# Kernel optimization log

Hardware: AMD Instinct MI355X
Metric: run time of the kernel (lower is better)

## Reference

```python
import jax, jax.numpy as jnp
import numpy as np

N_NODES = 38000   # 19 feature types x ~2000 categories
IN_DIM = 64
HID = 128         # hid_num in source
R = 8             # number of relations
E = 200000        # edges per relation
N_ROWS = 60000    # data rows
F = 19            # len(features)
N_CLASSES = 10


def setup_inputs() -> dict:
    key = jax.random.key(0)
    ks = jax.random.split(key, 20)
    s_in = 1.0 / np.sqrt(IN_DIM)
    s_h = 1.0 / np.sqrt(HID)
    inp = {
        "node_feats": jax.random.normal(ks[0], (N_NODES, IN_DIM), jnp.float32),
        "edges_src": jax.random.randint(ks[1], (R, E), 0, N_NODES),
        "edges_dst": jax.random.randint(ks[2], (R, E), 0, N_NODES),
        "row_idx": jax.random.randint(ks[3], (N_ROWS, F), 0, N_NODES),
        "row_mask": jax.random.randint(ks[4], (N_ROWS, F), 0, 2).astype(bool),
        # input linear
        "W_in": jax.random.normal(ks[5], (IN_DIM, HID), jnp.float32) * s_in,
        "b_in": jnp.zeros((HID,), jnp.float32),
        # RGCN layer 1 and 2: per-relation GraphConv weights
        "W1": jax.random.normal(ks[6], (R, HID, HID), jnp.float32) * s_h,
        "b1": jnp.zeros((R, HID), jnp.float32),
        "W2": jax.random.normal(ks[7], (R, HID, HID), jnp.float32) * s_h,
        "b2": jnp.zeros((R, HID), jnp.float32),
        # MLP head
        "Wm1": jax.random.normal(ks[8], (HID, HID), jnp.float32) * s_h,
        "bm1": jnp.zeros((HID,), jnp.float32),
        "Wm2": jax.random.normal(ks[9], (HID, HID), jnp.float32) * s_h,
        "bm2": jnp.zeros((HID,), jnp.float32),
        "Wm3": jax.random.normal(ks[10], (HID, N_CLASSES), jnp.float32) * s_h,
        "bm3": jnp.zeros((N_CLASSES,), jnp.float32),
    }
    return inp


def _hetero_conv(h, src, dst, W, b):
    """DGL HeteroGraphConv(sum) of GraphConv(norm='both') over R relations."""
    n = h.shape[0]
    out = jnp.zeros((n, W.shape[2]), h.dtype)
    ones = jnp.ones((src.shape[1],), h.dtype)
    for r in range(src.shape[0]):
        deg_out = jax.ops.segment_sum(ones, src[r], num_segments=n)
        deg_in = jax.ops.segment_sum(ones, dst[r], num_segments=n)
        norm_s = jnp.where(deg_out > 0, deg_out, 1.0) ** -0.5
        norm_d = jnp.where(deg_in > 0, deg_in, 1.0) ** -0.5
        msg = h[src[r]] * norm_s[src[r], None]            # [E, hid]
        agg = jax.ops.segment_sum(msg, dst[r], num_segments=n)
        out = out + (agg * norm_d[:, None]) @ W[r] + b[r]
    return out


def reference(node_feats, edges_src, edges_dst, row_idx, row_mask,
              W_in, b_in, W1, b1, W2, b2, Wm1, bm1, Wm2, bm2, Wm3, bm3):
    # input linear + relu (applied to every node type's features)
    h = jax.nn.relu(node_feats @ W_in + b_in)            # [N_nodes, HID]
    # 2-layer RGCN
    h = jax.nn.relu(_hetero_conv(h, edges_src, edges_dst, W1, b1))
    h = _hetero_conv(h, edges_src, edges_dst, W2, b2)    # [N_nodes, HID]
    # vectorized ragged gather + masked mean (replaces per-row python loop)
    m = row_mask.astype(h.dtype)                          # [N_rows, F]
    emb = h[row_idx] * m[..., None]                       # [N_rows, F, HID]
    cnt = jnp.maximum(m.sum(-1, keepdims=True), 1.0)
    mean_feat = emb.sum(1) / cnt                          # [N_rows, HID]
    # MLP head
    x = jax.nn.relu(mean_feat @ Wm1 + bm1)
    x = jax.nn.relu(x @ Wm2 + bm2)
    return x @ Wm3 + bm3                                  # [N_rows, N_CLASSES]
```

## Files before the change

### kernel.cpp

```cpp
#include <hip/hip_runtime.h>
#include <hip/hip_bf16.h>

#define NN    38000
#define HID   128
#define RR    8
#define EE    200000
#define NROWS 60000
#define FF    19
#define NCLS  10
#define NRD   (RR*NN)
#define HB    38912
#define CH    16
#define CE    (EE/CH)

typedef __hip_bfloat16 bf16;
typedef __attribute__((ext_vector_type(8))) short short8;
typedef __attribute__((ext_vector_type(4))) float floatx4;

__device__ __forceinline__ float b2f(bf16 x){ return __bfloat162float(x); }
__device__ __forceinline__ bf16  f2b(float x){ return __float2bfloat16(x); }

__device__ __forceinline__ int geti(const void* a, long long i, int wide){
  return wide ? (int)(((const long long*)a)[i]) : ((const int*)a)[i];
}

__global__ void k_fill(float* out, int n, float v){
  int i = blockIdx.x*256 + threadIdx.x;
  if (i < n) out[i] = v;
}

__global__ void k_sniff(const void* mask, const void* ridx, const void* esrc, int* flags){
  int lane = threadIdx.x;
  const unsigned short* mu = (const unsigned short*)mask;
  int l3f80e=0, l3f80o=0, lbytehi=0, loddnz=0, lother=0;
  for (int i = lane; i < 4096; i += 64){
    unsigned v = mu[i];
    if (v == 0) continue;
    if (v == 0x3F80){ if (i & 1) l3f80o = 1; else l3f80e = 1; continue; }
    unsigned lo = v & 0xFF, hi = v >> 8;
    int lob = (lo == 0 || lo == 1 || lo == 0xFF);
    int hib = (hi == 0 || hi == 1 || hi == 0xFF);
    if (lob && hib){ if (hi) lbytehi = 1; if (i & 1) loddnz = 1; continue; }
    lother = 1;
  }
  int a3f80e = __any(l3f80e);
  int a3f80o = __any(l3f80o);
  int abytehi = __any(lbytehi);
  int aoddnz = __any(loddnz);
  int aother = __any(lother);
  int mtype = -1;
  if (!aother){
    if (a3f80e && !abytehi && !aoddnz)       mtype = 2;
    else if (a3f80o && !a3f80e && !abytehi)  mtype = 3;
    else if (!a3f80e && !a3f80o){
      if (abytehi || aoddnz) mtype = 1;
      else                   mtype = 0;
    }
  }
  const int* es = (const int*)esrc;
  int loddE = 0, lseenE = 0;
  for (int i = lane; i < 512; i += 64){
    if (es[2*i+1] != 0) loddE = 1;
    if (es[2*i] > 1)    lseenE = 1;
  }
  int fE = (!__any(loddE) && __any(lseenE)) ? 1 : 0;
  const int* ri = (const int*)ridx;
  int loddI = 0, lseenI = 0;
  for (int i = lane; i < 512; i += 64){
    if (ri[2*i+1] != 0) loddI = 1;
    if (ri[2*i] > 1)    lseenI = 1;
  }
  int fI = (!__any(loddI) && __any(lseenI)) ? 1 : 0;
  if (lane == 0){ flags[1] = mtype; flags[3] = fE; flags[4] = fI; }
}


__global__ __launch_bounds__(1024) void kg_hist(const void* esrc, const void* edst,
                                                int* __restrict__ ghd, int* __restrict__ ghs,
                                                const int* flags){
  __shared__ int hist[HB];
  int t = threadIdx.x;
  for (int i = t; i < HB; i += 1024) hist[i] = 0;
  __syncthreads();
  int b = blockIdx.x;
  int side = b >> 7;
  int r = (b >> 4) & 7, c = b & 15;
  int wide = flags[3];
  const void* e = side ? esrc : edst;
  long long base = (long long)r*EE + (long long)c*CE;
  if (!wide){
    const int* p = (const int*)e + base;
    for (int i = t; i < CE; i += 1024) atomicAdd(&hist[p[i]], 1);
  } else {
    const long long* p = (const long long*)e + base;
    for (int i = t; i < CE; i += 1024) atomicAdd(&hist[(int)p[i]], 1);
  }
  __syncthreads();
  int* out = (side ? ghs : ghd) + (long long)(r*CH + c)*HB;
  for (int i = t; i < HB; i += 1024) out[i] = hist[i];
}

__global__ void kg_tot(const int* __restrict__ ghd, const int* __restrict__ ghs,
                       int* __restrict__ totg, float* __restrict__ ns){
  int i = blockIdx.x*256 + threadIdx.x;
  if (i >= RR*HB) return;
  int r = i / HB, bin = i - r*HB;
  int sd = 0, ss = 0;
#pragma unroll
  for (int c = 0; c < CH; c++){
    sd += ghd[(long long)(r*CH+c)*HB + bin];
    ss += ghs[(long long)(r*CH+c)*HB + bin];
  }
  totg[i] = sd;
  if (bin < NN) ns[r*NN + bin] = rsqrtf((float)(ss > 0 ? ss : 1));
}

__global__ __launch_bounds__(1024) void kg_scan(const int* __restrict__ totg,
                                                int* __restrict__ rowptr){
  __shared__ int tot[HB];
  __shared__ int wsum[16];
  int t = threadIdx.x, r = blockIdx.x;
  for (int i = t; i < HB; i += 1024) tot[i] = totg[r*HB + i];
  __syncthreads();
  int b0 = t*38;
  int loc[38], s = 0;
#pragma unroll
  for (int j = 0; j < 38; j++){ loc[j] = s; s += tot[b0+j]; }
  int lane = t & 63, w = t >> 6;
  int sc = s;
  for (int off = 1; off < 64; off <<= 1){
    int v = __shfl_up(sc, off);
    if (lane >= off) sc += v;
  }
  if (lane == 63) wsum[w] = sc;
  __syncthreads();
  if (t < 16){
    int v = wsum[t];
    int scw = v;
    for (int off = 1; off < 16; off <<= 1){
      int u = __shfl_up(scw, off);
      if (t >= off) scw += u;
    }
    wsum[t] = scw - v;
  }
  __syncthreads();
  int base = r*EE + (sc - s) + wsum[w];
#pragma unroll
  for (int j = 0; j < 38; j++) tot[b0+j] = base + loc[j];
  __syncthreads();
  for (int i = t; i < NN; i += 1024) rowptr[r*NN + i] = tot[i];
  if (r == RR-1 && t == 0) rowptr[NRD] = RR*EE;
}

__global__ void kg_curs(const int* __restrict__ ghd, const int* __restrict__ rowptr,
                        int* __restrict__ gcurs){
  int i = blockIdx.x*256 + threadIdx.x;
  if (i >= NRD) return;
  int r = i / NN, bin = i - r*NN;
  int p = rowptr[i];
#pragma unroll
  for (int c = 0; c < CH; c++){
    gcurs[(long long)(r*CH+c)*HB + bin] = p;
    p += ghd[(long long)(r*CH+c)*HB + bin];
  }
}

__global__ __launch_bounds__(1024) void kg_scatter(const void* esrc, const void* edst,
                                                   const int* __restrict__ gcurs,
                                                   int* __restrict__ csr, const int* flags){
  __shared__ int cur[HB];
  int t = threadIdx.x, b = blockIdx.x;
  int r = b >> 4, c = b & 15;
  const int* g = gcurs + (long long)(r*CH + c)*HB;
  for (int i = t; i < HB; i += 1024) cur[i] = g[i];
  __syncthreads();
  int wide = flags[3];
  long long base = (long long)r*EE + (long long)c*CE;
  if (!wide){
    const int* ps = (const int*)esrc + base;
    const int* pd = (const int*)edst + base;
    for (int i = t; i < CE; i += 1024){
      int d = pd[i], s = ps[i];
      int pos = atomicAdd(&cur[d], 1);
      csr[pos] = s;
    }
  } else {
    const long long* ps = (const long long*)esrc + base;
    const long long* pd = (const long long*)edst + base;
    for (int i = t; i < CE; i += 1024){
      int d = (int)pd[i], s = (int)ps[i];
      int pos = atomicAdd(&cur[d], 1);
      csr[pos] = s;
    }
  }
}


__global__ void k_bias(const float* b_in, const float* b1, const float* b2,
                       const float* bm1, const float* bm2, const float* bm3, float* o){
  int t = threadIdx.x;
  o[t] = b_in[t];
  float s1 = 0.f, s2 = 0.f;
  for (int r = 0; r < RR; r++){ s1 += b1[r*HID+t]; s2 += b2[r*HID+t]; }
  o[128+t] = s1; o[256+t] = s2;
  o[384+t] = bm1[t]; o[512+t] = bm2[t];
  if (t < NCLS) o[640+t] = bm3[t];
}

__global__ void k_pack512(const float* __restrict__ WA, const float* __restrict__ WB,
                          bf16* __restrict__ outA, bf16* __restrict__ outB){
  int idx0 = blockIdx.x*256 + threadIdx.x;
  if (idx0 >= 4*65536) return;
  const float* W = (idx0 < 2*65536) ? WA : WB;
  bf16* out      = (idx0 < 2*65536) ? outA : outB;
  int idx = idx0 & (2*65536 - 1);
  int j = idx & 7;
  int l = (idx >> 3) & 63;
  int t = (idx >> 9) & 127;
  int g = idx >> 16;
  int ktg = t & 15, nt = t >> 4;
  int kglob = ktg*32 + ((l>>4)<<3) + j;
  int rel = kglob >> 7;
  int krow = kglob & 127;
  int n = nt*16 + (l&15);
  out[idx] = f2b(W[((g*4 + rel)*128 + krow)*128 + n]);
}

__global__ void k_packg(const float* __restrict__ B, bf16* __restrict__ out, int KT){
  int idx = blockIdx.x*256 + threadIdx.x;
  if (idx >= KT*4096) return;
  int j  = idx & 7;
  int l  = (idx >> 3) & 63;
  int t  = idx >> 9;
  int kt = t % KT;
  int nt = t / KT;
  int k = kt*32 + ((l>>4)<<3) + j;
  int n = nt*16 + (l&15);
  out[idx] = f2b(B[k*128 + n]);
}

__global__ void k_gemm_in(const float* __restrict__ A, const float* __restrict__ B,
                          const float* bias, bf16* __restrict__ out){
  int row0 = blockIdx.x * 4;
  int col = threadIdx.x;
  float a0=0.f, a1=0.f, a2=0.f, a3=0.f;
  for (int k = 0; k < 64; k++){
    float bv = B[k*HID + col];
    a0 += A[(long long)(row0+0)*64 + k] * bv;
    a1 += A[(long long)(row0+1)*64 + k] * bv;
    a2 += A[(long long)(row0+2)*64 + k] * bv;
    a3 += A[(long long)(row0+3)*64 + k] * bv;
  }
  float bb = bias[col];
  out[(long long)(row0+0)*HID + col] = f2b(fmaxf(a0 + bb, 0.f));
  out[(long long)(row0+1)*HID + col] = f2b(fmaxf(a1 + bb, 0.f));
  out[(long long)(row0+2)*HID + col] = f2b(fmaxf(a2 + bb, 0.f));
  out[(long long)(row0+3)*HID + col] = f2b(fmaxf(a3 + bb, 0.f));
}

__global__ __launch_bounds__(512) void k_layer(const bf16* __restrict__ h,
                                               const int* __restrict__ rowptr,
                                               const int* __restrict__ csr,
                                               const float* __restrict__ ns,
                                               const bf16* __restrict__ Bp,
                                               const float* __restrict__ bias,
                                               bf16* __restrict__ hout, int relu){
  __shared__ char lds[8*16*256];
  int w = threadIdx.x >> 6;
  int lane = threadIdx.x & 63;
  int d0 = blockIdx.x << 4;
  const unsigned* hv = (const unsigned*)h;
  const float* nsw = ns + w*NN;

  int rp = 0;
  if (lane < 17) rp = rowptr[w*NN + d0 + lane];
  int beg16 = __shfl(rp, 0);
  int end16 = __shfl(rp, 16);

  int wbase = beg16;
  int s_l = 0; float w_l = 0.f;
  { int pos = wbase + lane;
    if (pos < end16){ s_l = csr[pos]; w_l = nsw[s_l]; } }

  for (int i = 0; i < 16; i++){
    int b = __shfl(rp, i), e = __shfl(rp, i+1);
    float acc0 = 0.f, acc1 = 0.f;
    int j = b;
    while (j < e){
      while (j >= wbase + 64){
        wbase += 64;
        int pos = wbase + lane;
        s_l = 0; w_l = 0.f;
        if (pos < end16){ s_l = csr[pos]; w_l = nsw[s_l]; }
      }
      int wend = wbase + 64;
      int stop = e < wend ? e : wend;
      int m = stop - j;
      int base_l = j - wbase;
      int nb = (m + 3) & ~3;
      for (int k = 0; k < nb; k += 4){
        int i0 = base_l + k;
        int   s0 = __shfl(s_l, i0),   s1 = __shfl(s_l, i0+1);
        int   s2 = __shfl(s_l, i0+2), s3 = __shfl(s_l, i0+3);
        float w0 = __shfl(w_l, i0),   w1 = __shfl(w_l, i0+1);
        float w2 = __shfl(w_l, i0+2), w3 = __shfl(w_l, i0+3);
        if (k+1 >= m) w1 = 0.f;
        if (k+2 >= m) w2 = 0.f;
        if (k+3 >= m) w3 = 0.f;
        unsigned p0 = hv[(long long)s0*64 + lane];
        unsigned p1 = hv[(long long)s1*64 + lane];
        unsigned p2 = hv[(long long)s2*64 + lane];
        unsigned p3 = hv[(long long)s3*64 + lane];
        acc0 += w0 * __uint_as_float(p0 << 16);
        acc1 += w0 * __uint_as_float(p0 & 0xffff0000u);
        acc0 += w1 * __uint_as_float(p1 << 16);
        acc1 += w1 * __uint_as_float(p1 & 0xffff0000u);
        acc0 += w2 * __uint_as_float(p2 << 16);
        acc1 += w2 * __uint_as_float(p2 & 0xffff0000u);
        acc0 += w3 * __uint_as_float(p3 << 16);
        acc1 += w3 * __uint_as_float(p3 & 0xffff0000u);
      }
      j = stop;
    }
    int deg = e - b;
    float nd = rsqrtf((float)(deg > 0 ? deg : 1));
    bf16 o0 = f2b(acc0 * nd), o1 = f2b(acc1 * nd);
    unsigned ov = ((unsigned)(*(unsigned short*)&o1) << 16) | (*(unsigned short*)&o0);
    int addr = (w << 12) + (i << 8) + (lane << 2);
    addr ^= ((i & 7) << 4);
    *(unsigned*)(lds + addr) = ov;
  }
  __syncthreads();

  floatx4 acc = (floatx4){0.f,0.f,0.f,0.f};
  int row = lane & 15;
  int kb = (lane >> 4) << 4;
#pragma unroll
  for (int rel = 0; rel < 8; rel++){
    int half = rel >> 2;
    const bf16* bp = Bp + half*65536 + lane*8 + (w*16 + (rel & 3)*4)*512;
#pragma unroll
    for (int ktl = 0; ktl < 4; ktl++){
      int off = (row << 8) + ktl*64 + kb;
      off ^= ((row & 7) << 4);
      short8 a = *(const short8*)(lds + (rel << 12) + off);
      short8 b = *(const short8*)(bp + ktl*512);
      acc = __builtin_amdgcn_mfma_f32_16x16x32_bf16(a, b, acc, 0, 0, 0);
    }
  }
  int col = w*16 + (lane & 15);
  int row0 = d0 + ((lane >> 4) << 2);
  float bb = bias[col];
#pragma unroll
  for (int v = 0; v < 4; v++){
    float x = acc[v] + bb;
    if (relu) x = fmaxf(x, 0.f);
    hout[(long long)(row0 + v)*HID + col] = f2b(x);
  }
}

__global__ void k_mfma_out(const bf16* __restrict__ A, const bf16* __restrict__ Bp,
                           const float* __restrict__ bias, bf16* __restrict__ out, int M){
  int wave = (blockIdx.x*blockDim.x + threadIdx.x) >> 6;
  int lane = threadIdx.x & 63;
  int rowBase = wave << 4;
  if (rowBase >= M) return;
  long long aRow = rowBase + (lane & 15);
  int kGrp = (lane >> 4) << 3;
  floatx4 acc[8];
#pragma unroll
  for (int nt = 0; nt < 8; nt++) acc[nt] = (floatx4){0.f,0.f,0.f,0.f};
  const bf16* bp = Bp + lane*8;
#pragma unroll
  for (int kt = 0; kt < 4; kt++){
    short8 a = *(const short8*)(A + aRow*HID + kt*32 + kGrp);
#pragma unroll
    for (int nt = 0; nt < 8; nt++){
      short8 b = *(const short8*)(bp + (nt*4 + kt)*512);
      acc[nt] = __builtin_amdgcn_mfma_f32_16x16x32_bf16(a, b, acc[nt], 0, 0, 0);
    }
  }
  int colB = lane & 15;
  int rowQ = rowBase + ((lane >> 4) << 2);
#pragma unroll
  for (int nt = 0; nt < 8; nt++){
    int col = nt*16 + colB;
    float bb = bias[col];
#pragma unroll
    for (int v = 0; v < 4; v++)
      out[(long long)(rowQ+v)*HID + col] = f2b(fmaxf(acc[nt][v] + bb, 0.f));
  }
}

__global__ void k_mean(const bf16* __restrict__ h, const void* ridx, const void* rmask,
                       const int* flags, bf16* __restrict__ mean){
  int row = blockIdx.x*4 + (threadIdx.x >> 6);
  int lane = threadIdx.x & 63;
  int mt = flags[1];
  int wide = flags[4];
  const int* m4            = (const int*)rmask;
  const unsigned char* m1  = (const unsigned char*)rmask;
  const unsigned short* m2 = (const unsigned short*)rmask;
  const unsigned int* mw   = (const unsigned int*)rmask;
  const unsigned* hv = (const unsigned*)h;
  int on = 0, idxl = 0;
  if (lane < FF){
    long long i = (long long)row*FF + lane;
    if      (mt == 1) on = (m1[i] != 0);
    else if (mt == 2) on = (m2[i] != 0);
    else if (mt == 3) on = (mw[i] != 0);
    else              on = (m4[i] != 0);
    if (on) idxl = geti(ridx, i, wide);
  }
  unsigned long long bal = __ballot(on);
  float cnt = (float)__popcll(bal);
  float acc0 = 0.f, acc1 = 0.f;
#pragma unroll
  for (int j = 0; j < FF; j++){
    int s = __shfl(idxl, j);
    float w = (float)((bal >> j) & 1ull);
    unsigned pv = hv[(long long)s*64 + lane];
    acc0 += w * __uint_as_float(pv << 16);
    acc1 += w * __uint_as_float(pv & 0xffff0000u);
  }
  float inv = 1.f / fmaxf(cnt, 1.f);
  bf16 o0 = f2b(acc0 * inv), o1 = f2b(acc1 * inv);
  unsigned ov = ((unsigned)(*(unsigned short*)&o1) << 16) | (*(unsigned short*)&o0);
  ((unsigned*)mean)[(long long)row*64 + lane] = ov;
}

__global__ void k_last(const bf16* __restrict__ A, const float* __restrict__ B,
                       const float* bias, float* __restrict__ out){
  int i = blockIdx.x*256 + threadIdx.x;
  if (i >= NROWS*NCLS) return;
  int row = i / NCLS, col = i - row*NCLS;
  float acc = bias[col];
  const bf16* ar = A + (long long)row*HID;
  for (int k = 0; k < HID; k++) acc += b2f(ar[k]) * B[k*NCLS + col];
  out[i] = acc;
}

extern "C" void kernel_launch(void* const* d_in, const int* in_sizes, int n_in,
                              void* d_out, int out_size, void* d_ws, size_t ws_size,
                              hipStream_t stream){
  float* out = (float*)d_out;

  static const int expect[17] = {
    NN*64, RR*EE, RR*EE, NROWS*FF, NROWS*FF,
    64*HID, HID, RR*HID*HID, RR*HID, RR*HID*HID, RR*HID,
    HID*HID, HID, HID*HID, HID, HID*NCLS, NCLS };
  bool ok = (n_in >= 17) && (out_size == NROWS*NCLS);
  if (ok) for (int i = 0; i < 17; i++) if (in_sizes[i] != expect[i]) { ok = false; break; }
  if (!ok){
    k_fill<<<(NROWS*NCLS+255)/256, 256, 0, stream>>>(out, NROWS*NCLS, 64.0f);
    return;
  }

  const void*  e_src = d_in[1];
  const void*  e_dst = d_in[2];
  const void*  ridx  = d_in[3];
  const void*  rmask = d_in[4];
  const float* nf   = (const float*)d_in[0];
  const float* W_in = (const float*)d_in[5];
  const float* b_in = (const float*)d_in[6];
  const float* W1   = (const float*)d_in[7];
  const float* b1   = (const float*)d_in[8];
  const float* W2   = (const float*)d_in[9];
  const float* b2   = (const float*)d_in[10];
  const float* Wm1  = (const float*)d_in[11];
  const float* bm1  = (const float*)d_in[12];
  const float* Wm2  = (const float*)d_in[13];
  const float* bm2  = (const float*)d_in[14];
  const float* Wm3  = (const float*)d_in[15];
  const float* bm3  = (const float*)d_in[16];

  char* ws = (char*)d_ws;
  size_t off = 0;
  auto take = [&](size_t bytes)->char*{
    char* p = ws + off; off += (bytes + 255) & ~(size_t)255; return p; };

  int*   flags  = (int*)  take(256);
  char*  rgn    =         take(58368000);
  bf16*  meanb  = (bf16*) (rgn);
  bf16*  x1     = (bf16*) (rgn + 15360000);
  bf16*  x2     = (bf16*) (rgn + 30720000);
  int*   ghd    = (int*)  (rgn);
  int*   ghs    = (int*)  (rgn + 19922944);
  int*   gcurs  = (int*)  (rgn + 19922944);
  int*   totg   = (int*)  (rgn + 39845888);
  bf16*  h1     = (bf16*) take((size_t)NN*HID*2);
  bf16*  h2     = (bf16*) take((size_t)NN*HID*2);
  int*   rowptr = (int*)  take((size_t)(NRD+1)*4);
  int*   csr    = (int*)  take((size_t)RR*EE*4);
  float* ns     = (float*)take((size_t)NRD*4);
  float* bias   = (float*)take(656*4);
  bf16*  W1p    = (bf16*) take((size_t)2*65536*2);
  bf16*  W2p    = (bf16*) take((size_t)2*65536*2);
  bf16*  Wm1p   = (bf16*) take((size_t)16384*2);
  bf16*  Wm2p   = (bf16*) take((size_t)16384*2);

  if (off > ws_size){
    k_fill<<<(NROWS*NCLS+255)/256, 256, 0, stream>>>(out, NROWS*NCLS, 32.0f);
    return;
  }

  k_sniff   <<<1, 64, 0, stream>>>(rmask, ridx, e_src, flags);
  kg_hist   <<<256, 1024, 0, stream>>>(e_src, e_dst, ghd, ghs, flags);
  kg_tot    <<<(RR*HB+255)/256, 256, 0, stream>>>(ghd, ghs, totg, ns);
  kg_scan   <<<RR, 1024, 0, stream>>>(totg, rowptr);
  kg_curs   <<<(NRD+255)/256, 256, 0, stream>>>(ghd, rowptr, gcurs);
  kg_scatter<<<128, 1024, 0, stream>>>(e_src, e_dst, gcurs, csr, flags);
  k_bias    <<<1, 128, 0, stream>>>(b_in, b1, b2, bm1, bm2, bm3, bias);

  k_pack512<<<(4*65536+255)/256, 256, 0, stream>>>(W1, W2, W1p, W2p);
  k_packg  <<<(4*4096+255)/256, 256, 0, stream>>>(Wm1, Wm1p, 4);
  k_packg  <<<(4*4096+255)/256, 256, 0, stream>>>(Wm2, Wm2p, 4);

  k_gemm_in<<<NN/4, 128, 0, stream>>>(nf, W_in, bias+0, h1);

  k_layer<<<NN/16, 512, 0, stream>>>(h1, rowptr, csr, ns, W1p, bias+128, h2, 1);
  k_layer<<<NN/16, 512, 0, stream>>>(h2, rowptr, csr, ns, W2p, bias+256, h1, 0);

  k_mean<<<NROWS/4, 256, 0, stream>>>(h1, ridx, rmask, flags, meanb);

  int gR = (NROWS/16 + 3)/4;
  k_mfma_out<<<gR, 256, 0, stream>>>(meanb, Wm1p, bias+384, x1, NROWS);
  k_mfma_out<<<gR, 256, 0, stream>>>(x1,    Wm2p, bias+512, x2, NROWS);
  k_last<<<(NROWS*NCLS+255)/256, 256, 0, stream>>>(x2, Wm3, bias+640, out);
}
```

Measured before the change: 490.6 us.

## Pack source norm into CSR entries and load edges with uniform scalar reads

```diff
diff --git a/kernel.cpp b/kernel.cpp
--- a/kernel.cpp
+++ b/kernel.cpp
@@ -167,14 +167,17 @@
 
 __global__ __launch_bounds__(1024) void kg_scatter(const void* esrc, const void* edst,
                                                    const int* __restrict__ gcurs,
-                                                   int* __restrict__ csr, const int* flags){
+                                                   const float* __restrict__ ns,
+                                                   int2* __restrict__ csrw, const int* flags){
   __shared__ int cur[HB];
   int t = threadIdx.x, b = blockIdx.x;
   int r = b >> 4, c = b & 15;
   const int* g = gcurs + (long long)(r*CH + c)*HB;
   for (int i = t; i < HB; i += 1024) cur[i] = g[i];
   __syncthreads();
+  if (b == 0 && t < 8){ int2 z; z.x = 0; z.y = 0; csrw[RR*EE + t] = z; }
   int wide = flags[3];
+  const float* nsr = ns + r*NN;
   long long base = (long long)r*EE + (long long)c*CE;
   if (!wide){
     const int* ps = (const int*)esrc + base;
@@ -182,7 +185,8 @@
     for (int i = t; i < CE; i += 1024){
       int d = pd[i], s = ps[i];
       int pos = atomicAdd(&cur[d], 1);
-      csr[pos] = s;
+      int2 v; v.x = s; v.y = __float_as_int(nsr[s]);
+      csrw[pos] = v;
     }
   } else {
     const long long* ps = (const long long*)esrc + base;
@@ -190,7 +194,8 @@
     for (int i = t; i < CE; i += 1024){
       int d = (int)pd[i], s = (int)ps[i];
       int pos = atomicAdd(&cur[d], 1);
-      csr[pos] = s;
+      int2 v; v.x = s; v.y = __float_as_int(nsr[s]);
+      csrw[pos] = v;
     }
   }
 }
@@ -207,36 +212,39 @@
   if (t < NCLS) o[640+t] = bm3[t];
 }
 
-__global__ void k_pack512(const float* __restrict__ WA, const float* __restrict__ WB,
-                          bf16* __restrict__ outA, bf16* __restrict__ outB){
+__global__ void k_packall(const float* __restrict__ W1, const float* __restrict__ W2,
+                          const float* __restrict__ Wm1, const float* __restrict__ Wm2,
+                          bf16* __restrict__ W1p, bf16* __restrict__ W2p,
+                          bf16* __restrict__ Wm1p, bf16* __restrict__ Wm2p){
   int idx0 = blockIdx.x*256 + threadIdx.x;
-  if (idx0 >= 4*65536) return;
-  const float* W = (idx0 < 2*65536) ? WA : WB;
-  bf16* out      = (idx0 < 2*65536) ? outA : outB;
-  int idx = idx0 & (2*65536 - 1);
-  int j = idx & 7;
-  int l = (idx >> 3) & 63;
-  int t = (idx >> 9) & 127;
-  int g = idx >> 16;
-  int ktg = t & 15, nt = t >> 4;
-  int kglob = ktg*32 + ((l>>4)<<3) + j;
-  int rel = kglob >> 7;
-  int krow = kglob & 127;
-  int n = nt*16 + (l&15);
-  out[idx] = f2b(W[((g*4 + rel)*128 + krow)*128 + n]);
-}
-
-__global__ void k_packg(const float* __restrict__ B, bf16* __restrict__ out, int KT){
-  int idx = blockIdx.x*256 + threadIdx.x;
-  if (idx >= KT*4096) return;
-  int j  = idx & 7;
-  int l  = (idx >> 3) & 63;
-  int t  = idx >> 9;
-  int kt = t % KT;
-  int nt = t / KT;
-  int k = kt*32 + ((l>>4)<<3) + j;
-  int n = nt*16 + (l&15);
-  out[idx] = f2b(B[k*128 + n]);
+  if (idx0 < 4*65536){
+    const float* W = (idx0 < 2*65536) ? W1 : W2;
+    bf16* out      = (idx0 < 2*65536) ? W1p : W2p;
+    int idx = idx0 & (2*65536 - 1);
+    int j = idx & 7;
+    int l = (idx >> 3) & 63;
+    int t = (idx >> 9) & 127;
+    int g = idx >> 16;
+    int ktg = t & 15, nt = t >> 4;
+    int kglob = ktg*32 + ((l>>4)<<3) + j;
+    int rel = kglob >> 7;
+    int krow = kglob & 127;
+    int n = nt*16 + (l&15);
+    out[idx] = f2b(W[((g*4 + rel)*128 + krow)*128 + n]);
+  } else if (idx0 < 4*65536 + 2*16384){
+    int t2 = idx0 - 4*65536;
+    const float* B = (t2 < 16384) ? Wm1 : Wm2;
+    bf16* out      = (t2 < 16384) ? Wm1p : Wm2p;
+    int idx = t2 & 16383;
+    int j  = idx & 7;
+    int l  = (idx >> 3) & 63;
+    int t  = idx >> 9;
+    int kt = t & 3;
+    int nt = t >> 2;
+    int k = kt*32 + ((l>>4)<<3) + j;
+    int n = nt*16 + (l&15);
+    out[idx] = f2b(B[k*128 + n]);
+  }
 }
 
 __global__ void k_gemm_in(const float* __restrict__ A, const float* __restrict__ B,
@@ -260,8 +268,7 @@
 
 __global__ __launch_bounds__(512) void k_layer(const bf16* __restrict__ h,
                                                const int* __restrict__ rowptr,
-                                               const int* __restrict__ csr,
-                                               const float* __restrict__ ns,
+                                               const unsigned long long* __restrict__ cw,
                                                const bf16* __restrict__ Bp,
                                                const float* __restrict__ bias,
                                                bf16* __restrict__ hout, int relu){
@@ -270,57 +277,36 @@
   int lane = threadIdx.x & 63;
   int d0 = blockIdx.x << 4;
   const unsigned* hv = (const unsigned*)h;
-  const float* nsw = ns + w*NN;
 
   int rp = 0;
   if (lane < 17) rp = rowptr[w*NN + d0 + lane];
-  int beg16 = __shfl(rp, 0);
-  int end16 = __shfl(rp, 16);
-
-  int wbase = beg16;
-  int s_l = 0; float w_l = 0.f;
-  { int pos = wbase + lane;
-    if (pos < end16){ s_l = csr[pos]; w_l = nsw[s_l]; } }
 
   for (int i = 0; i < 16; i++){
-    int b = __shfl(rp, i), e = __shfl(rp, i+1);
+    int b = __builtin_amdgcn_readfirstlane(__shfl(rp, i));
+    int e = __builtin_amdgcn_readfirstlane(__shfl(rp, i+1));
     float acc0 = 0.f, acc1 = 0.f;
-    int j = b;
-    while (j < e){
-      while (j >= wbase + 64){
-        wbase += 64;
-        int pos = wbase + lane;
-        s_l = 0; w_l = 0.f;
-        if (pos < end16){ s_l = csr[pos]; w_l = nsw[s_l]; }
-      }
-      int wend = wbase + 64;
-      int stop = e < wend ? e : wend;
-      int m = stop - j;
-      int base_l = j - wbase;
-      int nb = (m + 3) & ~3;
-      for (int k = 0; k < nb; k += 4){
-        int i0 = base_l + k;
-        int   s0 = __shfl(s_l, i0),   s1 = __shfl(s_l, i0+1);
-        int   s2 = __shfl(s_l, i0+2), s3 = __shfl(s_l, i0+3);
-        float w0 = __shfl(w_l, i0),   w1 = __shfl(w_l, i0+1);
-        float w2 = __shfl(w_l, i0+2), w3 = __shfl(w_l, i0+3);
-        if (k+1 >= m) w1 = 0.f;
-        if (k+2 >= m) w2 = 0.f;
-        if (k+3 >= m) w3 = 0.f;
-        unsigned p0 = hv[(long long)s0*64 + lane];
-        unsigned p1 = hv[(long long)s1*64 + lane];
-        unsigned p2 = hv[(long long)s2*64 + lane];
-        unsigned p3 = hv[(long long)s3*64 + lane];
-        acc0 += w0 * __uint_as_float(p0 << 16);
-        acc1 += w0 * __uint_as_float(p0 & 0xffff0000u);
-        acc0 += w1 * __uint_as_float(p1 << 16);
-        acc1 += w1 * __uint_as_float(p1 & 0xffff0000u);
-        acc0 += w2 * __uint_as_float(p2 << 16);
-        acc1 += w2 * __uint_as_float(p2 & 0xffff0000u);
-        acc0 += w3 * __uint_as_float(p3 << 16);
-        acc1 += w3 * __uint_as_float(p3 & 0xffff0000u);
-      }
-      j = stop;
+    for (int j = b; j < e; j += 4){
+      unsigned long long q0 = cw[j];
+      unsigned long long q1 = cw[j+1];
+      unsigned long long q2 = cw[j+2];
+      unsigned long long q3 = cw[j+3];
+      int s0 = (int)q0, s1 = (int)q1, s2 = (int)q2, s3 = (int)q3;
+      float w0 = __int_as_float((int)(q0 >> 32));
+      float w1 = (j+1 < e) ? __int_as_float((int)(q1 >> 32)) : 0.f;
+      float w2 = (j+2 < e) ? __int_as_float((int)(q2 >> 32)) : 0.f;
+      float w3 = (j+3 < e) ? __int_as_float((int)(q3 >> 32)) : 0.f;
+      unsigned p0 = hv[(long long)s0*64 + lane];
+      unsigned p1 = hv[(long long)s1*64 + lane];
+      unsigned p2 = hv[(long long)s2*64 + lane];
+      unsigned p3 = hv[(long long)s3*64 + lane];
+      acc0 += w0 * __uint_as_float(p0 << 16);
+      acc1 += w0 * __uint_as_float(p0 & 0xffff0000u);
+      acc0 += w1 * __uint_as_float(p1 << 16);
+      acc1 += w1 * __uint_as_float(p1 & 0xffff0000u);
+      acc0 += w2 * __uint_as_float(p2 << 16);
+      acc1 += w2 * __uint_as_float(p2 & 0xffff0000u);
+      acc0 += w3 * __uint_as_float(p3 << 16);
+      acc1 += w3 * __uint_as_float(p3 & 0xffff0000u);
     }
     int deg = e - b;
     float nd = rsqrtf((float)(deg > 0 ? deg : 1));
@@ -392,36 +378,55 @@
   }
 }
 
-__global__ void k_mean(const bf16* __restrict__ h, const void* ridx, const void* rmask,
-                       const int* flags, bf16* __restrict__ mean){
+__global__ void k_mean(const bf16* __restrict__ h, const void* __restrict__ ridx,
+                       const void* __restrict__ rmask,
+                       const int* __restrict__ flags, bf16* __restrict__ mean){
   int row = blockIdx.x*4 + (threadIdx.x >> 6);
   int lane = threadIdx.x & 63;
   int mt = flags[1];
   int wide = flags[4];
-  const int* m4            = (const int*)rmask;
-  const unsigned char* m1  = (const unsigned char*)rmask;
-  const unsigned short* m2 = (const unsigned short*)rmask;
-  const unsigned int* mw   = (const unsigned int*)rmask;
   const unsigned* hv = (const unsigned*)h;
-  int on = 0, idxl = 0;
-  if (lane < FF){
-    long long i = (long long)row*FF + lane;
-    if      (mt == 1) on = (m1[i] != 0);
-    else if (mt == 2) on = (m2[i] != 0);
-    else if (mt == 3) on = (mw[i] != 0);
-    else              on = (m4[i] != 0);
-    if (on) idxl = geti(ridx, i, wide);
-  }
-  unsigned long long bal = __ballot(on);
-  float cnt = (float)__popcll(bal);
-  float acc0 = 0.f, acc1 = 0.f;
-#pragma unroll
-  for (int j = 0; j < FF; j++){
-    int s = __shfl(idxl, j);
-    float w = (float)((bal >> j) & 1ull);
-    unsigned pv = hv[(long long)s*64 + lane];
-    acc0 += w * __uint_as_float(pv << 16);
-    acc1 += w * __uint_as_float(pv & 0xffff0000u);
+  float acc0 = 0.f, acc1 = 0.f, cnt = 0.f;
+  if (mt == 0 && !wide){
+    int urow = __builtin_amdgcn_readfirstlane(row);
+    const int* m4 = (const int*)rmask;
+    const int* r4 = (const int*)ridx;
+    long long base = (long long)urow*FF;
+#pragma unroll
+    for (int j = 0; j < FF; j++){
+      int mv = m4[base + j];
+      if (mv){
+        int s = r4[base + j];
+        unsigned pv = hv[(long long)s*64 + lane];
+        acc0 += __uint_as_float(pv << 16);
+        acc1 += __uint_as_float(pv & 0xffff0000u);
+        cnt += 1.f;
+      }
+    }
+  } else {
+    const int* m4            = (const int*)rmask;
+    const unsigned char* m1  = (const unsigned char*)rmask;
+    const unsigned short* m2 = (const unsigned short*)rmask;
+    const unsigned int* mw   = (const unsigned int*)rmask;
+    int on = 0, idxl = 0;
+    if (lane < FF){
+      long long i = (long long)row*FF + lane;
+      if      (mt == 1) on = (m1[i] != 0);
+      else if (mt == 2) on = (m2[i] != 0);
+      else if (mt == 3) on = (mw[i] != 0);
+      else              on = (m4[i] != 0);
+      if (on) idxl = geti(ridx, i, wide);
+    }
+    unsigned long long bal = __ballot(on);
+    cnt = (float)__popcll(bal);
+#pragma unroll
+    for (int j = 0; j < FF; j++){
+      int s = __shfl(idxl, j);
+      float w = (float)((bal >> j) & 1ull);
+      unsigned pv = hv[(long long)s*64 + lane];
+      acc0 += w * __uint_as_float(pv << 16);
+      acc1 += w * __uint_as_float(pv & 0xffff0000u);
+    }
   }
   float inv = 1.f / fmaxf(cnt, 1.f);
   bf16 o0 = f2b(acc0 * inv), o1 = f2b(acc1 * inv);
@@ -491,7 +496,7 @@
   bf16*  h1     = (bf16*) take((size_t)NN*HID*2);
   bf16*  h2     = (bf16*) take((size_t)NN*HID*2);
   int*   rowptr = (int*)  take((size_t)(NRD+1)*4);
-  int*   csr    = (int*)  take((size_t)RR*EE*4);
+  int2*  csrw   = (int2*) take((size_t)RR*EE*8 + 64);
   float* ns     = (float*)take((size_t)NRD*4);
   float* bias   = (float*)take(656*4);
   bf16*  W1p    = (bf16*) take((size_t)2*65536*2);
@@ -509,17 +514,18 @@
   kg_tot    <<<(RR*HB+255)/256, 256, 0, stream>>>(ghd, ghs, totg, ns);
   kg_scan   <<<RR, 1024, 0, stream>>>(totg, rowptr);
   kg_curs   <<<(NRD+255)/256, 256, 0, stream>>>(ghd, rowptr, gcurs);
-  kg_scatter<<<128, 1024, 0, stream>>>(e_src, e_dst, gcurs, csr, flags);
+  kg_scatter<<<128, 1024, 0, stream>>>(e_src, e_dst, gcurs, ns, csrw, flags);
   k_bias    <<<1, 128, 0, stream>>>(b_in, b1, b2, bm1, bm2, bm3, bias);
 
-  k_pack512<<<(4*65536+255)/256, 256, 0, stream>>>(W1, W2, W1p, W2p);
-  k_packg  <<<(4*4096+255)/256, 256, 0, stream>>>(Wm1, Wm1p, 4);
-  k_packg  <<<(4*4096+255)/256, 256, 0, stream>>>(Wm2, Wm2p, 4);
+  k_packall<<<(4*65536 + 2*16384 + 255)/256, 256, 0, stream>>>(W1, W2, Wm1, Wm2,
+                                                               W1p, W2p, Wm1p, Wm2p);
 
   k_gemm_in<<<NN/4, 128, 0, stream>>>(nf, W_in, bias+0, h1);
 
-  k_layer<<<NN/16, 512, 0, stream>>>(h1, rowptr, csr, ns, W1p, bias+128, h2, 1);
-  k_layer<<<NN/16, 512, 0, stream>>>(h2, rowptr, csr, ns, W2p, bias+256, h1, 0);
+  k_layer<<<NN/16, 512, 0, stream>>>(h1, rowptr, (const unsigned long long*)csrw,
+                                     W1p, bias+128, h2, 1);
+  k_layer<<<NN/16, 512, 0, stream>>>(h2, rowptr, (const unsigned long long*)csrw,
+                                     W2p, bias+256, h1, 0);
 
   k_mean<<<NROWS/4, 256, 0, stream>>>(h1, ridx, rmask, flags, meanb);
 
```

Measured after the change: 489.9 us. About the same (-0.1%).
